# Optimization experiments

Hardware: AMD Instinct MI355X
Metric: run time of the kernel (lower is better)

The kernel has to match this reference:

```python
import jax, jax.numpy as jnp
import numpy as np

B, N, NUM_CLASS = 32, 4096, 40


def setup_inputs() -> dict:
    key = jax.random.key(0)
    ks = jax.random.split(key, 16)
    def w(k, o, i):
        return (jax.random.normal(k, (o, i), jnp.float32) / np.float32(np.sqrt(i)))
    inp = {"x": jax.random.uniform(ks[0], (B, N, 3), jnp.float32)}
    dims = [("sa1", 3, [64, 64, 128]), ("sa2", 3 + 128, [128, 128, 256]), ("sa3", 3 + 256, [256, 512, 1024])]
    ki = 1
    for name, cin, hs in dims:
        c = cin
        for j, h in enumerate(hs):
            inp[f"{name}_w{j}"] = w(jax.random.fold_in(ks[ki], j), h, c)
            inp[f"{name}_b{j}"] = jnp.zeros((h,), jnp.float32)
            c = h
        ki += 1
    for name, o, i in [("fc1", 512, 1024), ("fc2", 256, 512), ("fc3", NUM_CLASS, 256)]:
        inp[f"{name}_w"] = w(ks[ki], o, i)
        inp[f"{name}_b"] = jnp.zeros((o,), jnp.float32)
        ki += 1
    return inp


def _fps(xyz, npoint):
    # farthest point sampling for a single cloud, xyz: [N, 3] -> [npoint] indices
    n = xyz.shape[0]
    def body(carry, _):
        mind, last = carry
        d = jnp.sum((xyz - xyz[last]) ** 2, axis=-1)
        mind = jnp.minimum(mind, d)
        return (mind, jnp.argmax(mind).astype(jnp.int32)), last
    init = (jnp.full((n,), 1e10, xyz.dtype), jnp.int32(0))
    _, idx = jax.lax.scan(body, init, None, length=npoint)
    return idx


def _ball_query(new_xyz, xyz, radius, nsample):
    # new_xyz: [B,S,3], xyz: [B,N,3] -> [B,S,nsample] neighbor indices
    n = xyz.shape[1]
    sqd = (jnp.sum(new_xyz ** 2, -1)[:, :, None]
           + jnp.sum(xyz ** 2, -1)[:, None, :]
           - 2.0 * jnp.einsum('bsc,bnc->bsn', new_xyz, xyz))  # [B,S,N]
    gid = jnp.where(sqd <= radius ** 2, jnp.arange(n, dtype=jnp.int32), jnp.int32(n))
    gid = jnp.sort(gid, axis=-1)[..., :nsample]
    first = gid[..., :1]
    return jnp.where(gid == n, first, gid)


def _gather(x, idx):
    # x: [B,N,C], idx: [B,S,K] -> [B,S,K,C]
    return jax.vmap(lambda xb, ib: xb[ib])(x, idx)


def _shared_mlp(feat, layers):
    # feat: [..., C_in]; layers: list of (W [C_out,C_in], b [C_out]); 1x1 conv + ReLU (BN folded)
    for W, b in layers:
        feat = jax.nn.relu(jnp.einsum('bskc,oc->bsko', feat, W) + b)
    return feat


def _set_abstraction(xyz, feat, npoint, radius, nsample, layers):
    fidx = jax.vmap(lambda p: _fps(p, npoint))(xyz)            # [B,S]
    new_xyz = jax.vmap(lambda p, i: p[i])(xyz, fidx)           # [B,S,3]
    idx = _ball_query(new_xyz, xyz, radius, nsample)           # [B,S,K]
    gxyz = _gather(xyz, idx) - new_xyz[:, :, None, :]          # relative coords
    g = gxyz if feat is None else jnp.concatenate([gxyz, _gather(feat, idx)], axis=-1)
    g = _shared_mlp(g, layers)
    return new_xyz, jnp.max(g, axis=2)                         # max-pool over ball


def _sa_group_all(xyz, feat, layers):
    g = jnp.concatenate([xyz, feat], axis=-1)[:, None]         # [B,1,N,3+C]
    g = _shared_mlp(g, layers)
    return jnp.max(g, axis=2)[:, 0]                            # [B, 1024]


def reference(x,
              sa1_w0, sa1_b0, sa1_w1, sa1_b1, sa1_w2, sa1_b2,
              sa2_w0, sa2_b0, sa2_w1, sa2_b1, sa2_w2, sa2_b2,
              sa3_w0, sa3_b0, sa3_w1, sa3_b1, sa3_w2, sa3_b2,
              fc1_w, fc1_b, fc2_w, fc2_b, fc3_w, fc3_b):
    xyz, feat = x, None
    xyz, feat = _set_abstraction(xyz, feat, 512, 0.2, 32,
                                 [(sa1_w0, sa1_b0), (sa1_w1, sa1_b1), (sa1_w2, sa1_b2)])
    xyz, feat = _set_abstraction(xyz, feat, 128, 0.4, 64,
                                 [(sa2_w0, sa2_b0), (sa2_w1, sa2_b1), (sa2_w2, sa2_b2)])
    feat = _sa_group_all(xyz, feat,
                         [(sa3_w0, sa3_b0), (sa3_w1, sa3_b1), (sa3_w2, sa3_b2)])
    h = jax.nn.relu(feat @ fc1_w.T + fc1_b)
    h = jax.nn.relu(h @ fc2_w.T + fc2_b)
    logits = h @ fc3_w.T + fc3_b
    return jax.nn.softmax(logits, axis=-1)  # eval-mode output
```

## Files before the change

kernel.cpp:

```cpp
#include <hip/hip_runtime.h>
#include <math.h>

#define B_ 32
#define N_ 4096

typedef __attribute__((ext_vector_type(8))) short short8;
typedef __attribute__((ext_vector_type(4))) float f32x4;

__device__ __forceinline__ unsigned short f2bf(float f) {
    unsigned u = __float_as_uint(f);
    unsigned r = 0x7FFFu + ((u >> 16) & 1u);
    return (unsigned short)((u + r) >> 16);
}
__device__ __forceinline__ float bf2f(unsigned short h) {
    return __uint_as_float(((unsigned)h) << 16);
}
__device__ __forceinline__ void f2bfpair(float v, short& h, short& l) {
    unsigned short hh = f2bf(v);
    h = (short)hh;
    l = (short)f2bf(v - bf2f(hh));
}

__device__ __forceinline__ unsigned long long u64max(unsigned long long a,
                                                     unsigned long long b) {
    return a > b ? a : b;
}
template<int CTRL>
__device__ __forceinline__ unsigned long long dpp_u64(unsigned long long k) {
    int lo = __builtin_amdgcn_mov_dpp((int)(unsigned)k, CTRL, 0xf, 0xf, true);
    int hi = __builtin_amdgcn_mov_dpp((int)(unsigned)(k >> 32), CTRL, 0xf, 0xf, true);
    return ((unsigned long long)(unsigned)hi << 32) | (unsigned)lo;
}
__device__ __forceinline__ unsigned long long wave_argmax_u64(unsigned long long key) {
    key = u64max(key, dpp_u64<0x128>(key));
    key = u64max(key, dpp_u64<0x124>(key));
    key = u64max(key, dpp_u64<0x122>(key));
    key = u64max(key, dpp_u64<0x121>(key));
    key = u64max(key, __shfl_xor(key, 16));
    key = u64max(key, __shfl_xor(key, 32));
    return key;
}
__device__ __forceinline__ unsigned long long wave_argmax_u64_leader(unsigned long long key) {
    key = u64max(key, dpp_u64<0x128>(key));
    key = u64max(key, dpp_u64<0x124>(key));
    key = u64max(key, dpp_u64<0x122>(key));
    key = u64max(key, dpp_u64<0x121>(key));
    key = u64max(key, dpp_u64<0x142>(key));
    key = u64max(key, dpp_u64<0x143>(key));
    return key;
}

template<int N, int NPOINT, int NT>
__global__ __launch_bounds__(NT, 1) void fps_kernel(
    const float* __restrict__ xyz,
    int* __restrict__ outIdx,
    float* __restrict__ outXyz) {
#pragma clang fp contract(off)
    const int b = blockIdx.x;
    const int t = threadIdx.x;
    constexpr int PPT = N / NT;
    constexpr int NW = (NT + 63) / 64;
    __shared__ float ps[N][4];
    __shared__ unsigned long long red[2][NW];
    const float* base = xyz + (size_t)b * N * 3;
    for (int j = t; j < N; j += NT) {
        ps[j][0] = base[j * 3 + 0];
        ps[j][1] = base[j * 3 + 1];
        ps[j][2] = base[j * 3 + 2];
    }
    __syncthreads();
    float px[PPT], py[PPT], pz[PPT], mind[PPT];
    unsigned notp[PPT];
#pragma unroll
    for (int i = 0; i < PPT; i++) {
        int p = t + i * NT;
        f32x4 c4 = *(const f32x4*)&ps[p][0];
        px[i] = c4[0]; py[i] = c4[1]; pz[i] = c4[2];
        mind[i] = 1e10f;
        notp[i] = ~(unsigned)p;
    }
#pragma unroll
    for (int i = 0; i < PPT; i++)
        asm volatile("" : "+v"(px[i]), "+v"(py[i]), "+v"(pz[i]));
    float lx = ps[0][0], ly = ps[0][1], lz = ps[0][2];
    if (t == 0) {
        outIdx[b * NPOINT] = 0;
        outXyz[(size_t)b * NPOINT * 3 + 0] = lx;
        outXyz[(size_t)b * NPOINT * 3 + 1] = ly;
        outXyz[(size_t)b * NPOINT * 3 + 2] = lz;
    }
    for (int it = 1; it < NPOINT; it++) {
        unsigned long long key = 0;
#pragma unroll
        for (int i = 0; i < PPT; i++) {
            float dx = px[i] - lx, dy = py[i] - ly, dz = pz[i] - lz;
            float t0 = dx * dx, t1 = dy * dy, t2 = dz * dz;
            float d = (t0 + t1) + t2;
            float m = fminf(mind[i], d);
            mind[i] = m;
            unsigned long long k =
                ((unsigned long long)__float_as_uint(m) << 32) | notp[i];
            key = u64max(key, k);
        }
        int fi;
        if constexpr (NT > 64) {
            key = wave_argmax_u64_leader(key);
            const int par = it & 1;
            if ((t & 63) == 63) red[par][t >> 6] = key;
            __syncthreads();
            unsigned long long best = red[par][0];
#pragma unroll
            for (int w = 1; w < NW; w++) best = u64max(best, red[par][w]);
            fi = (int)(~(unsigned)best);
        } else {
            key = wave_argmax_u64(key);
            fi = (int)(~(unsigned)key);
        }
        f32x4 c4 = *(const f32x4*)&ps[fi][0];
        lx = c4[0]; ly = c4[1]; lz = c4[2];
        if (t == 0) {
            outIdx[b * NPOINT + it] = fi;
            outXyz[((size_t)b * NPOINT + it) * 3 + 0] = lx;
            outXyz[((size_t)b * NPOINT + it) * 3 + 1] = ly;
            outXyz[((size_t)b * NPOINT + it) * 3 + 2] = lz;
        }
    }
}

template<int N, int NS>
__global__ __launch_bounds__(256) void ballquery_kernel(
    const float* __restrict__ xyz, const float* __restrict__ newXyz,
    int* __restrict__ outIdx, int S, float r2) {
#pragma clang fp contract(off)
    const int qid = blockIdx.x * 4 + (threadIdx.x >> 6);
    const int lane = threadIdx.x & 63;
    const int b = qid / S;
    const float* q = newXyz + (size_t)qid * 3;
    const float qx = q[0], qy = q[1], qz = q[2];
    const float qn = (qx * qx + qy * qy) + qz * qz;
    const float* base = xyz + (size_t)b * N * 3;
    int* dst = outIdx + (size_t)qid * NS;
    int cnt = 0, first = 0;
    for (int p0 = 0; p0 < N; p0 += 64) {
        const int p = p0 + lane;
        const float x = base[p * 3 + 0];
        const float y = base[p * 3 + 1];
        const float z = base[p * 3 + 2];
        const float pn = (x * x + y * y) + z * z;
        const float dot = (qx * x + qy * y) + qz * z;
        const float sqd = (qn + pn) - 2.0f * dot;
        const unsigned long long mask = __ballot(sqd <= r2);
        if (mask) {
            if (cnt == 0) first = p0 + __ffsll((unsigned long long)mask) - 1;
            const int prefix = __builtin_amdgcn_mbcnt_hi(
                (unsigned)(mask >> 32),
                __builtin_amdgcn_mbcnt_lo((unsigned)mask, 0));
            const bool in = (mask >> lane) & 1ull;
            const int pos = cnt + prefix;
            if (in && pos < NS) dst[pos] = p;
            cnt += __popcll(mask);
            if (cnt >= NS) break;
        }
    }
    for (int i = cnt + lane; i < NS; i += 64) dst[i] = first;
}

struct WDesc { const float* src; short* dh; short* dl; int R, C, Cp, blk0, perm; };
struct WDescs { WDesc d[8]; };

__global__ void wprep_all_kernel(WDescs W) {
    const int blk = blockIdx.x;
    int di = 0;
#pragma unroll
    for (int k = 1; k < 8; k++) di = (blk >= W.d[k].blk0) ? k : di;
    const WDesc D = W.d[di];
    const int i = (blk - D.blk0) * 256 + threadIdx.x;
    if (i >= D.R * D.Cp) return;
    const int r = i / D.Cp, c = i % D.Cp;
    int cs;
    if (D.perm) cs = (c < 128) ? c + 3 : (c < 131 ? c - 128 : -1);
    else        cs = (c < D.C) ? c : -1;
    float v = (cs >= 0) ? D.src[r * D.C + cs] : 0.f;
    short h, l;
    f2bfpair(v, h, l);
    D.dh[i] = h; D.dl[i] = l;
}

template<int NT, int KS>
__device__ __forceinline__ void mfma_layer(
    const short* Aph, const short* Apl, const int sA,
    const short* __restrict__ Wph, const short* __restrict__ Wpl, const int sW,
    f32x4* acc, const int n0, const int mh, const int lr, const int lq) {
#pragma unroll
    for (int ks = 0; ks < KS; ks++) {
        const int ka = ks * 32 + lq * 8;
        short8 a_h[2], a_l[2];
#pragma unroll
        for (int mt = 0; mt < 2; mt++) {
            const int m = (mh * 2 + mt) * 16 + lr;
            a_h[mt] = *(const short8*)(Aph + m * sA + ka);
            a_l[mt] = *(const short8*)(Apl + m * sA + ka);
        }
#pragma unroll
        for (int nt = 0; nt < NT; nt++) {
            const int n = n0 + nt * 16 + lr;
            short8 b_h = *(const short8*)(Wph + (size_t)n * sW + ka);
            short8 b_l = *(const short8*)(Wpl + (size_t)n * sW + ka);
#pragma unroll
            for (int mt = 0; mt < 2; mt++) {
                f32x4 c = acc[mt * NT + nt];
                c = __builtin_amdgcn_mfma_f32_16x16x32_bf16(a_h[mt], b_h, c, 0, 0, 0);
                c = __builtin_amdgcn_mfma_f32_16x16x32_bf16(a_h[mt], b_l, c, 0, 0, 0);
                c = __builtin_amdgcn_mfma_f32_16x16x32_bf16(a_l[mt], b_h, c, 0, 0, 0);
                acc[mt * NT + nt] = c;
            }
        }
    }
}

template<int NT>
__device__ __forceinline__ void init_bias(f32x4* acc, const float* __restrict__ bias,
                                          const int n0, const int lr) {
#pragma unroll
    for (int nt = 0; nt < NT; nt++) {
        float bv = bias[n0 + nt * 16 + lr];
        f32x4 c = {bv, bv, bv, bv};
        acc[0 * NT + nt] = c;
        acc[1 * NT + nt] = c;
    }
}

template<int NT>
__device__ __forceinline__ void store_split(
    const f32x4* acc, short* Hp, short* Lp, const int stride,
    const int n0, const int mh, const int lr, const int lq) {
#pragma unroll
    for (int mt = 0; mt < 2; mt++)
#pragma unroll
        for (int nt = 0; nt < NT; nt++)
#pragma unroll
            for (int r = 0; r < 4; r++) {
                float v = fmaxf(acc[mt * NT + nt][r], 0.f);
                short h, l;
                f2bfpair(v, h, l);
                const int m = (mh * 2 + mt) * 16 + lq * 4 + r;
                const int n = n0 + nt * 16 + lr;
                Hp[m * stride + n] = h;
                Lp[m * stride + n] = l;
            }
}

#define T1 72
__global__ __launch_bounds__(256) void sa1_mfma_kernel(
    const float* __restrict__ x, const float* __restrict__ nxyz1,
    const int* __restrict__ idx,
    const float* __restrict__ w0, const float* __restrict__ b0,
    const short* __restrict__ w1h, const short* __restrict__ w1l,
    const float* __restrict__ b1,
    const short* __restrict__ w2h, const short* __restrict__ w2l,
    const float* __restrict__ b2,
    short* __restrict__ feat1h, short* __restrict__ feat1l) {
    const int g0 = blockIdx.x * 2;
    const int b = g0 >> 9;
    const int t = threadIdx.x;
    const int lane = t & 63, wv = t >> 6;
    const int lr = lane & 15, lq = lane >> 4;
    const int mh = wv & 1, nh = wv >> 1;
    __shared__ float gx[64][4];
    __shared__ short H1h[64 * T1], H1l[64 * T1];
    __shared__ short H2h[64 * T1], H2l[64 * T1];
    if (t < 64) {
        int g = g0 + (t >> 5);
        int id = idx[(size_t)g * 32 + (t & 31)];
        const float* pp = x + ((size_t)b * N_ + id) * 3;
        const float* cc = nxyz1 + (size_t)g * 3;
        gx[t][0] = pp[0] - cc[0];
        gx[t][1] = pp[1] - cc[1];
        gx[t][2] = pp[2] - cc[2];
    }
    __syncthreads();
    {
        const int m = t >> 2, oc = (t & 3) * 16;
        float a0 = gx[m][0], a1 = gx[m][1], a2 = gx[m][2];
        short8 hv0, hv1, lv0, lv1;
#pragma unroll
        for (int i = 0; i < 16; i++) {
            int o = oc + i;
            float v = fmaf(w0[o * 3 + 0], a0,
                      fmaf(w0[o * 3 + 1], a1,
                      fmaf(w0[o * 3 + 2], a2, b0[o])));
            v = fmaxf(v, 0.f);
            short h, l;
            f2bfpair(v, h, l);
            if (i < 8) { hv0[i] = h; lv0[i] = l; }
            else       { hv1[i - 8] = h; lv1[i - 8] = l; }
        }
        *(short8*)&H1h[m * T1 + oc]     = hv0;
        *(short8*)&H1h[m * T1 + oc + 8] = hv1;
        *(short8*)&H1l[m * T1 + oc]     = lv0;
        *(short8*)&H1l[m * T1 + oc + 8] = lv1;
    }
    __syncthreads();
    {
        f32x4 acc[4];
        init_bias<2>(acc, b1, nh * 32, lr);
        mfma_layer<2, 2>(H1h, H1l, T1, w1h, w1l, 64, acc, nh * 32, mh, lr, lq);
        store_split<2>(acc, H2h, H2l, T1, nh * 32, mh, lr, lq);
    }
    __syncthreads();
    {
        f32x4 acc[8];
        init_bias<4>(acc, b2, nh * 64, lr);
        mfma_layer<4, 2>(H2h, H2l, T1, w2h, w2l, 64, acc, nh * 64, mh, lr, lq);
#pragma unroll
        for (int nt = 0; nt < 4; nt++) {
            float v = 0.f;
#pragma unroll
            for (int mt = 0; mt < 2; mt++)
#pragma unroll
                for (int r = 0; r < 4; r++)
                    v = fmaxf(v, acc[mt * 4 + nt][r]);
            v = fmaxf(v, __shfl_xor(v, 16));
            v = fmaxf(v, __shfl_xor(v, 32));
            if (lane < 16) {
                short h, l;
                f2bfpair(v, h, l);
                size_t o = (size_t)(g0 + mh) * 128 + nh * 64 + nt * 16 + lane;
                feat1h[o] = h;
                feat1l[o] = l;
            }
        }
    }
}

#define S1 168
#define S2 136
__global__ __launch_bounds__(256) void sa2_mfma_kernel(
    const float* __restrict__ xyz1,
    const short* __restrict__ feat1h, const short* __restrict__ feat1l,
    const float* __restrict__ newXyz, const int* __restrict__ idx,
    const short* __restrict__ w0h, const short* __restrict__ w0l,
    const float* __restrict__ b0,
    const short* __restrict__ w1h, const short* __restrict__ w1l,
    const float* __restrict__ b1,
    const short* __restrict__ w2h, const short* __restrict__ w2l,
    const float* __restrict__ b2,
    short* __restrict__ a3h, short* __restrict__ a3l) {
    const int g = blockIdx.x;
    const int b = g >> 7;
    const int t = threadIdx.x;
    const int lane = t & 63, wv = t >> 6;
    const int lr = lane & 15, lq = lane >> 4;
    const int mh = wv & 1, nh = wv >> 1;
    __shared__ short Ah[64 * S1], Al[64 * S1];
    __shared__ short Hh[64 * S2], Hl[64 * S2];
    __shared__ float pmax[2][256];
    __shared__ int ids[64];
    if (t < 64) ids[t] = idx[(size_t)g * 64 + t];
    __syncthreads();
    {
        const int m = t >> 2, q = t & 3;
        const int id = ids[m];
        const size_t frow = ((size_t)b * 512 + id) * 128;
#pragma unroll
        for (int c8 = 0; c8 < 4; c8++) {
            const int k = q * 32 + c8 * 8;
            *(short8*)&Ah[m * S1 + k] = *(const short8*)(feat1h + frow + k);
            *(short8*)&Al[m * S1 + k] = *(const short8*)(feat1l + frow + k);
        }
        if (t < 64) {
            const int id2 = ids[t];
            short8 zz = {0, 0, 0, 0, 0, 0, 0, 0};
            *(short8*)&Ah[t * S1 + 128] = zz;
            *(short8*)&Ah[t * S1 + 136] = zz;
            *(short8*)&Ah[t * S1 + 144] = zz;
            *(short8*)&Ah[t * S1 + 152] = zz;
            *(short8*)&Al[t * S1 + 128] = zz;
            *(short8*)&Al[t * S1 + 136] = zz;
            *(short8*)&Al[t * S1 + 144] = zz;
            *(short8*)&Al[t * S1 + 152] = zz;
            const float* prow = xyz1 + ((size_t)b * 512 + id2) * 3;
            const float* crow = newXyz + (size_t)g * 3;
#pragma unroll
            for (int c = 0; c < 3; c++) {
                short h, l;
                f2bfpair(prow[c] - crow[c], h, l);
                Ah[t * S1 + 128 + c] = h;
                Al[t * S1 + 128 + c] = l;
            }
        }
    }
    __syncthreads();
    {
        f32x4 acc[8];
        init_bias<4>(acc, b0, nh * 64, lr);
        mfma_layer<4, 5>(Ah, Al, S1, w0h, w0l, 160, acc, nh * 64, mh, lr, lq);
        store_split<4>(acc, Hh, Hl, S2, nh * 64, mh, lr, lq);
    }
    __syncthreads();
    {
        f32x4 acc[8];
        init_bias<4>(acc, b1, nh * 64, lr);
        mfma_layer<4, 4>(Hh, Hl, S2, w1h, w1l, 128, acc, nh * 64, mh, lr, lq);
        store_split<4>(acc, Ah, Al, S2, nh * 64, mh, lr, lq);
    }
    __syncthreads();
    {
        f32x4 acc[16];
        init_bias<8>(acc, b2, nh * 128, lr);
        mfma_layer<8, 4>(Ah, Al, S2, w2h, w2l, 128, acc, nh * 128, mh, lr, lq);
#pragma unroll
        for (int nt = 0; nt < 8; nt++) {
            float v = 0.f;
#pragma unroll
            for (int mt = 0; mt < 2; mt++)
#pragma unroll
                for (int r = 0; r < 4; r++)
                    v = fmaxf(v, acc[mt * 8 + nt][r]);
            v = fmaxf(v, __shfl_xor(v, 16));
            v = fmaxf(v, __shfl_xor(v, 32));
            if (lane < 16) pmax[mh][nh * 128 + nt * 16 + lane] = v;
        }
    }
    __syncthreads();
    {
        float v = fmaxf(pmax[0][t], pmax[1][t]);
        short h, l;
        f2bfpair(v, h, l);
        a3h[(size_t)g * 288 + 3 + t] = h;
        a3l[(size_t)g * 288 + 3 + t] = l;
        if (t < 3) {
            f2bfpair(newXyz[(size_t)g * 3 + t], h, l);
            a3h[(size_t)g * 288 + t] = h;
            a3l[(size_t)g * 288 + t] = l;
        }
        if (t >= 227) {
            a3h[(size_t)g * 288 + t + 32] = 0;
            a3l[(size_t)g * 288 + t + 32] = 0;
        }
    }
}

template<int OUT_MODE>
__global__ __launch_bounds__(256) void mfma_gemm_kernel(
    const short* __restrict__ Agh, const short* __restrict__ Agl, const int Kp,
    const short* __restrict__ Wh, const short* __restrict__ Wl,
    const float* __restrict__ bias,
    float* __restrict__ outF, short* __restrict__ outH,
    short* __restrict__ outL, const int N) {
    const int t = threadIdx.x;
    const int lane = t & 63, wv = t >> 6;
    const int lr = lane & 15, lq = lane >> 4;
    const int mh = wv & 1, nh = wv >> 1;
    const int m0 = blockIdx.y * 64;
    const int n0 = blockIdx.x * 128 + nh * 64;
    __shared__ short Ah[64 * 40], Al[64 * 40];
    f32x4 acc[8];
#pragma unroll
    for (int nt = 0; nt < 4; nt++) {
        float bv = bias[n0 + nt * 16 + lr];
        f32x4 c = {bv, bv, bv, bv};
        acc[nt] = c; acc[4 + nt] = c;
    }
    const int srow = t >> 2, sk = (t & 3) * 8;
    for (int kt = 0; kt < Kp; kt += 32) {
        {
            const size_t src = (size_t)(m0 + srow) * Kp + kt + sk;
            *(short8*)&Ah[srow * 40 + sk] = *(const short8*)(Agh + src);
            *(short8*)&Al[srow * 40 + sk] = *(const short8*)(Agl + src);
        }
        __syncthreads();
        short8 a_h[2], a_l[2];
#pragma unroll
        for (int mt = 0; mt < 2; mt++) {
            const int m = mh * 32 + mt * 16 + lr;
            a_h[mt] = *(const short8*)&Ah[m * 40 + lq * 8];
            a_l[mt] = *(const short8*)&Al[m * 40 + lq * 8];
        }
#pragma unroll
        for (int nt = 0; nt < 4; nt++) {
            const int n = n0 + nt * 16 + lr;
            short8 b_h = *(const short8*)(Wh + (size_t)n * Kp + kt + lq * 8);
            short8 b_l = *(const short8*)(Wl + (size_t)n * Kp + kt + lq * 8);
#pragma unroll
            for (int mt = 0; mt < 2; mt++) {
                f32x4 c = acc[mt * 4 + nt];
                c = __builtin_amdgcn_mfma_f32_16x16x32_bf16(a_h[mt], b_h, c, 0, 0, 0);
                c = __builtin_amdgcn_mfma_f32_16x16x32_bf16(a_h[mt], b_l, c, 0, 0, 0);
                c = __builtin_amdgcn_mfma_f32_16x16x32_bf16(a_l[mt], b_h, c, 0, 0, 0);
                acc[mt * 4 + nt] = c;
            }
        }
        __syncthreads();
    }
    if (OUT_MODE == 2) {
        const int batch = blockIdx.y >> 1;
#pragma unroll
        for (int nt = 0; nt < 4; nt++) {
            float v = 0.f;
#pragma unroll
            for (int mt = 0; mt < 2; mt++)
#pragma unroll
                for (int r = 0; r < 4; r++)
                    v = fmaxf(v, acc[mt * 4 + nt][r]);
            v = fmaxf(v, __shfl_xor(v, 16));
            v = fmaxf(v, __shfl_xor(v, 32));
            if (lane < 16)
                atomicMax((int*)&outF[(size_t)batch * N + n0 + nt * 16 + lane],
                          __float_as_int(v));
        }
        return;
    }
#pragma unroll
    for (int mt = 0; mt < 2; mt++)
#pragma unroll
        for (int nt = 0; nt < 4; nt++)
#pragma unroll
            for (int r = 0; r < 4; r++) {
                const int m = m0 + mh * 32 + mt * 16 + lq * 4 + r;
                const int n = n0 + nt * 16 + lr;
                float v = fmaxf(acc[mt * 4 + nt][r], 0.f);
                short h, l;
                f2bfpair(v, h, l);
                outH[(size_t)m * N + n] = h;
                outL[(size_t)m * N + n] = l;
            }
}

template<int K, int OPW, int ACT>
__global__ __launch_bounds__(256) void fc_kernel(
    const float* __restrict__ in, const float* __restrict__ w,
    const float* __restrict__ bias, float* __restrict__ out, const int O) {
    const int batch = blockIdx.y;
    const int t = threadIdx.x, lane = t & 63, wv = t >> 6;
    __shared__ float f[K];
    for (int j = t; j < K; j += 256) f[j] = in[batch * K + j];
    __syncthreads();
    const int o0 = blockIdx.x * (4 * OPW) + wv * OPW;
#pragma unroll
    for (int i = 0; i < OPW; i++) {
        const int o = o0 + i;
        const float* wr = w + (size_t)o * K;
        float a = 0.f;
#pragma unroll
        for (int c = lane; c < K; c += 64) a = fmaf(wr[c], f[c], a);
#pragma unroll
        for (int off = 32; off > 0; off >>= 1) a += __shfl_xor(a, off);
        if (lane == 0) {
            float v = a + bias[o];
            out[batch * O + o] = ACT ? fmaxf(v, 0.f) : v;
        }
    }
}

__global__ __launch_bounds__(256) void fc3_softmax_kernel(
    const float* __restrict__ in, const float* __restrict__ w3,
    const float* __restrict__ b3, float* __restrict__ out) {
    const int b = blockIdx.x, t = threadIdx.x, lane = t & 63, wv = t >> 6;
    __shared__ float f[256];
    __shared__ float lg[40];
    f[t] = in[b * 256 + t];
    __syncthreads();
#pragma unroll
    for (int i = 0; i < 10; i++) {
        const int o = wv * 10 + i;
        const float* wr = w3 + (size_t)o * 256;
        float a = 0.f;
#pragma unroll
        for (int c = lane; c < 256; c += 64) a = fmaf(wr[c], f[c], a);
#pragma unroll
        for (int off = 32; off > 0; off >>= 1) a += __shfl_xor(a, off);
        if (lane == 0) lg[o] = a + b3[o];
    }
    __syncthreads();
    if (t < 64) {
        float v = (t < 40) ? lg[t] : -INFINITY;
        float m = v;
#pragma unroll
        for (int off = 32; off > 0; off >>= 1) m = fmaxf(m, __shfl_xor(m, off));
        float e = (t < 40) ? expf(v - m) : 0.f;
        float s = e;
#pragma unroll
        for (int off = 32; off > 0; off >>= 1) s += __shfl_xor(s, off);
        if (t < 40) out[b * 40 + t] = e / s;
    }
}

extern "C" void kernel_launch(void* const* d_in, const int* in_sizes, int n_in,
                              void* d_out, int out_size, void* d_ws, size_t ws_size,
                              hipStream_t stream) {
    (void)in_sizes; (void)n_in; (void)out_size; (void)ws_size;
    const float* x      = (const float*)d_in[0];
    const float* sa1w0  = (const float*)d_in[1];
    const float* sa1b0  = (const float*)d_in[2];
    const float* sa1w1  = (const float*)d_in[3];
    const float* sa1b1  = (const float*)d_in[4];
    const float* sa1w2  = (const float*)d_in[5];
    const float* sa1b2  = (const float*)d_in[6];
    const float* sa2w0  = (const float*)d_in[7];
    const float* sa2b0  = (const float*)d_in[8];
    const float* sa2w1  = (const float*)d_in[9];
    const float* sa2b1  = (const float*)d_in[10];
    const float* sa2w2  = (const float*)d_in[11];
    const float* sa2b2  = (const float*)d_in[12];
    const float* sa3w0  = (const float*)d_in[13];
    const float* sa3b0  = (const float*)d_in[14];
    const float* sa3w1  = (const float*)d_in[15];
    const float* sa3b1  = (const float*)d_in[16];
    const float* sa3w2  = (const float*)d_in[17];
    const float* sa3b2  = (const float*)d_in[18];
    const float* fc1w   = (const float*)d_in[19];
    const float* fc1b   = (const float*)d_in[20];
    const float* fc2w   = (const float*)d_in[21];
    const float* fc2b   = (const float*)d_in[22];
    const float* fc3w   = (const float*)d_in[23];
    const float* fc3b   = (const float*)d_in[24];
    float* outp = (float*)d_out;

    char* ws = (char*)d_ws;
    size_t off = 0;
    auto alloc = [&](size_t bytes) {
        void* p = ws + off;
        off += (bytes + 255) & ~(size_t)255;
        return p;
    };
    int*   fidx1   = (int*)  alloc((size_t)B_ * 512 * 4);
    float* nxyz1   = (float*)alloc((size_t)B_ * 512 * 3 * 4);
    int*   idx1    = (int*)  alloc((size_t)B_ * 512 * 32 * 4);
    short* feat1h  = (short*)alloc((size_t)B_ * 512 * 128 * 2);
    short* feat1l  = (short*)alloc((size_t)B_ * 512 * 128 * 2);
    int*   fidx2   = (int*)  alloc((size_t)B_ * 128 * 4);
    float* nxyz2   = (float*)alloc((size_t)B_ * 128 * 3 * 4);
    int*   idx2    = (int*)  alloc((size_t)B_ * 128 * 64 * 4);
    short* a3h     = (short*)alloc((size_t)4096 * 288 * 2);
    short* a3l     = (short*)alloc((size_t)4096 * 288 * 2);
    short* h3ah    = (short*)alloc((size_t)4096 * 256 * 2);
    short* h3al    = (short*)alloc((size_t)4096 * 256 * 2);
    short* h3bh    = (short*)alloc((size_t)4096 * 512 * 2);
    short* h3bl    = (short*)alloc((size_t)4096 * 512 * 2);
    float* gfeat   = (float*)alloc((size_t)B_ * 1024 * 4);
    float* h1      = (float*)alloc((size_t)B_ * 512 * 4);
    float* h2      = (float*)alloc((size_t)B_ * 256 * 4);
    short* w1h_s1 = (short*)alloc((size_t)64 * 64 * 2);
    short* w1l_s1 = (short*)alloc((size_t)64 * 64 * 2);
    short* w2h_s1 = (short*)alloc((size_t)128 * 64 * 2);
    short* w2l_s1 = (short*)alloc((size_t)128 * 64 * 2);
    short* w0h_s2 = (short*)alloc((size_t)128 * 160 * 2);
    short* w0l_s2 = (short*)alloc((size_t)128 * 160 * 2);
    short* w1h_s2 = (short*)alloc((size_t)128 * 128 * 2);
    short* w1l_s2 = (short*)alloc((size_t)128 * 128 * 2);
    short* w2h_s2 = (short*)alloc((size_t)256 * 128 * 2);
    short* w2l_s2 = (short*)alloc((size_t)256 * 128 * 2);
    short* w0h_s3 = (short*)alloc((size_t)256 * 288 * 2);
    short* w0l_s3 = (short*)alloc((size_t)256 * 288 * 2);
    short* w1h_s3 = (short*)alloc((size_t)512 * 256 * 2);
    short* w1l_s3 = (short*)alloc((size_t)512 * 256 * 2);
    short* w2h_s3 = (short*)alloc((size_t)1024 * 512 * 2);
    short* w2l_s3 = (short*)alloc((size_t)1024 * 512 * 2);

    {
        WDescs W;
        const float* srcs[8] = {sa1w1, sa1w2, sa2w0, sa2w1, sa2w2, sa3w0, sa3w1, sa3w2};
        short* dhs[8] = {w1h_s1, w2h_s1, w0h_s2, w1h_s2, w2h_s2, w0h_s3, w1h_s3, w2h_s3};
        short* dls[8] = {w1l_s1, w2l_s1, w0l_s2, w1l_s2, w2l_s2, w0l_s3, w1l_s3, w2l_s3};
        int Rs[8]  = {64, 128, 128, 128, 256, 256, 512, 1024};
        int Cs[8]  = {64, 64, 131, 128, 128, 259, 256, 512};
        int Cps[8] = {64, 64, 160, 128, 128, 288, 256, 512};
        int blk = 0;
        for (int k = 0; k < 8; k++) {
            W.d[k] = {srcs[k], dhs[k], dls[k], Rs[k], Cs[k], Cps[k], blk,
                      (k == 2) ? 1 : 0};
            blk += (Rs[k] * Cps[k] + 255) / 256;
        }
        wprep_all_kernel<<<blk, 256, 0, stream>>>(W);
    }
    hipMemsetAsync(gfeat, 0, (size_t)B_ * 1024 * 4, stream);

    fps_kernel<4096, 512, 256><<<B_, 256, 0, stream>>>(x, fidx1, nxyz1);
    ballquery_kernel<4096, 32><<<B_ * 512 / 4, 256, 0, stream>>>(
        x, nxyz1, idx1, 512, 0.04f);
    sa1_mfma_kernel<<<B_ * 512 / 2, 256, 0, stream>>>(
        x, nxyz1, idx1, sa1w0, sa1b0,
        w1h_s1, w1l_s1, sa1b1, w2h_s1, w2l_s1, sa1b2, feat1h, feat1l);
    fps_kernel<512, 128, 64><<<B_, 64, 0, stream>>>(nxyz1, fidx2, nxyz2);
    ballquery_kernel<512, 64><<<B_ * 128 / 4, 256, 0, stream>>>(
        nxyz1, nxyz2, idx2, 128, 0.16f);
    sa2_mfma_kernel<<<B_ * 128, 256, 0, stream>>>(
        nxyz1, feat1h, feat1l, nxyz2, idx2,
        w0h_s2, w0l_s2, sa2b0, w1h_s2, w1l_s2, sa2b1, w2h_s2, w2l_s2, sa2b2,
        a3h, a3l);
    mfma_gemm_kernel<1><<<dim3(2, 64), 256, 0, stream>>>(
        a3h, a3l, 288, w0h_s3, w0l_s3, sa3b0, nullptr, h3ah, h3al, 256);
    mfma_gemm_kernel<1><<<dim3(4, 64), 256, 0, stream>>>(
        h3ah, h3al, 256, w1h_s3, w1l_s3, sa3b1, nullptr, h3bh, h3bl, 512);
    mfma_gemm_kernel<2><<<dim3(8, 64), 256, 0, stream>>>(
        h3bh, h3bl, 512, w2h_s3, w2l_s3, sa3b2, gfeat, nullptr, nullptr, 1024);
    fc_kernel<1024, 16, 1><<<dim3(8, B_), 256, 0, stream>>>(
        gfeat, fc1w, fc1b, h1, 512);
    fc_kernel<512, 16, 1><<<dim3(4, B_), 256, 0, stream>>>(
        h1, fc2w, fc2b, h2, 256);
    fc3_softmax_kernel<<<B_, 256, 0, stream>>>(h2, fc3w, fc3b, outp);
}
```

Measured before the change: 1.032 ms.

## Co-schedule ball queries with second FPS and SA1 MLP in merged launches

The second-stage farthest point sampling only depends on the first FPS output, so it now runs as extra blocks of the first ball-query launch. The second ball query runs as extra blocks of the SA1 MLP launch. This removes two kernel launches and lets the serial, low-occupancy FPS2 overlap with independent ball-query and MLP work. Unused index outputs from FPS are also dropped. The cost is heterogeneous blocks inside one launch and a larger shared-memory footprint for the ball-query blocks, which may reduce occupancy.

```diff
diff --git a/kernel.cpp b/kernel.cpp
--- a/kernel.cpp
+++ b/kernel.cpp
@@ -52,9 +52,7 @@
 
 template<int N, int NPOINT, int NT>
 __global__ __launch_bounds__(NT, 1) void fps_kernel(
-    const float* __restrict__ xyz,
-    int* __restrict__ outIdx,
-    float* __restrict__ outXyz) {
+    const float* __restrict__ xyz, float* __restrict__ outXyz) {
 #pragma clang fp contract(off)
     const int b = blockIdx.x;
     const int t = threadIdx.x;
@@ -84,7 +82,6 @@
         asm volatile("" : "+v"(px[i]), "+v"(py[i]), "+v"(pz[i]));
     float lx = ps[0][0], ly = ps[0][1], lz = ps[0][2];
     if (t == 0) {
-        outIdx[b * NPOINT] = 0;
         outXyz[(size_t)b * NPOINT * 3 + 0] = lx;
         outXyz[(size_t)b * NPOINT * 3 + 1] = ly;
         outXyz[(size_t)b * NPOINT * 3 + 2] = lz;
@@ -102,24 +99,17 @@
                 ((unsigned long long)__float_as_uint(m) << 32) | notp[i];
             key = u64max(key, k);
         }
-        int fi;
-        if constexpr (NT > 64) {
-            key = wave_argmax_u64_leader(key);
-            const int par = it & 1;
-            if ((t & 63) == 63) red[par][t >> 6] = key;
-            __syncthreads();
-            unsigned long long best = red[par][0];
-#pragma unroll
-            for (int w = 1; w < NW; w++) best = u64max(best, red[par][w]);
-            fi = (int)(~(unsigned)best);
-        } else {
-            key = wave_argmax_u64(key);
-            fi = (int)(~(unsigned)key);
-        }
+        key = wave_argmax_u64_leader(key);
+        const int par = it & 1;
+        if ((t & 63) == 63) red[par][t >> 6] = key;
+        __syncthreads();
+        unsigned long long best = red[par][0];
+#pragma unroll
+        for (int w = 1; w < NW; w++) best = u64max(best, red[par][w]);
+        const int fi = (int)(~(unsigned)best);
         f32x4 c4 = *(const f32x4*)&ps[fi][0];
         lx = c4[0]; ly = c4[1]; lz = c4[2];
         if (t == 0) {
-            outIdx[b * NPOINT + it] = fi;
             outXyz[((size_t)b * NPOINT + it) * 3 + 0] = lx;
             outXyz[((size_t)b * NPOINT + it) * 3 + 1] = ly;
             outXyz[((size_t)b * NPOINT + it) * 3 + 2] = lz;
@@ -128,12 +118,10 @@
 }
 
 template<int N, int NS>
-__global__ __launch_bounds__(256) void ballquery_kernel(
+__device__ __forceinline__ void ballquery_body(
     const float* __restrict__ xyz, const float* __restrict__ newXyz,
-    int* __restrict__ outIdx, int S, float r2) {
+    int* __restrict__ outIdx, int S, float r2, int qid, int lane) {
 #pragma clang fp contract(off)
-    const int qid = blockIdx.x * 4 + (threadIdx.x >> 6);
-    const int lane = threadIdx.x & 63;
     const int b = qid / S;
     const float* q = newXyz + (size_t)qid * 3;
     const float qx = q[0], qy = q[1], qz = q[2];
@@ -165,6 +153,71 @@
     for (int i = cnt + lane; i < NS; i += 64) dst[i] = first;
 }
 
+template<int BQB, int NQ, int NS, int SQ, int NF, int NPF>
+__global__ __launch_bounds__(256) void bq_fps_kernel(
+    const float* __restrict__ xyzQ, const float* __restrict__ newXyzQ,
+    int* __restrict__ outIdxQ, float r2,
+    const float* __restrict__ xyzF, float* __restrict__ outXyzF) {
+#pragma clang fp contract(off)
+    const int t = threadIdx.x;
+    const int lane = t & 63, wv = t >> 6;
+    __shared__ float ps[NF][4];
+    if (blockIdx.x < BQB) {
+        ballquery_body<NQ, NS>(xyzQ, newXyzQ, outIdxQ, SQ, r2,
+                               blockIdx.x * 4 + wv, lane);
+        return;
+    }
+    const int b = blockIdx.x - BQB;
+    const float* base = xyzF + (size_t)b * NF * 3;
+    for (int j = t; j < NF; j += 256) {
+        ps[j][0] = base[j * 3 + 0];
+        ps[j][1] = base[j * 3 + 1];
+        ps[j][2] = base[j * 3 + 2];
+    }
+    __syncthreads();
+    if (t >= 64) return;
+    constexpr int PPT = NF / 64;
+    float px[PPT], py[PPT], pz[PPT], mind[PPT];
+    unsigned notp[PPT];
+#pragma unroll
+    for (int i = 0; i < PPT; i++) {
+        int p = t + i * 64;
+        f32x4 c4 = *(const f32x4*)&ps[p][0];
+        px[i] = c4[0]; py[i] = c4[1]; pz[i] = c4[2];
+        mind[i] = 1e10f;
+        notp[i] = ~(unsigned)p;
+    }
+    float lx = ps[0][0], ly = ps[0][1], lz = ps[0][2];
+    if (t == 0) {
+        outXyzF[(size_t)b * NPF * 3 + 0] = lx;
+        outXyzF[(size_t)b * NPF * 3 + 1] = ly;
+        outXyzF[(size_t)b * NPF * 3 + 2] = lz;
+    }
+    for (int it = 1; it < NPF; it++) {
+        unsigned long long key = 0;
+#pragma unroll
+        for (int i = 0; i < PPT; i++) {
+            float dx = px[i] - lx, dy = py[i] - ly, dz = pz[i] - lz;
+            float t0 = dx * dx, t1 = dy * dy, t2 = dz * dz;
+            float d = (t0 + t1) + t2;
+            float m = fminf(mind[i], d);
+            mind[i] = m;
+            unsigned long long k =
+                ((unsigned long long)__float_as_uint(m) << 32) | notp[i];
+            key = u64max(key, k);
+        }
+        key = wave_argmax_u64(key);
+        const int fi = (int)(~(unsigned)key);
+        f32x4 c4 = *(const f32x4*)&ps[fi][0];
+        lx = c4[0]; ly = c4[1]; lz = c4[2];
+        if (t == 0) {
+            outXyzF[((size_t)b * NPF + it) * 3 + 0] = lx;
+            outXyzF[((size_t)b * NPF + it) * 3 + 1] = ly;
+            outXyzF[((size_t)b * NPF + it) * 3 + 2] = lz;
+        }
+    }
+}
+
 struct WDesc { const float* src; short* dh; short* dl; int R, C, Cp, blk0, perm; };
 struct WDescs { WDesc d[8]; };
 
@@ -251,7 +304,8 @@
 }
 
 #define T1 72
-__global__ __launch_bounds__(256) void sa1_mfma_kernel(
+template<int SAB>
+__global__ __launch_bounds__(256) void sa1_bq2_kernel(
     const float* __restrict__ x, const float* __restrict__ nxyz1,
     const int* __restrict__ idx,
     const float* __restrict__ w0, const float* __restrict__ b0,
@@ -259,11 +313,17 @@
     const float* __restrict__ b1,
     const short* __restrict__ w2h, const short* __restrict__ w2l,
     const float* __restrict__ b2,
-    short* __restrict__ feat1h, short* __restrict__ feat1l) {
+    short* __restrict__ feat1h, short* __restrict__ feat1l,
+    const float* __restrict__ nxyz2, int* __restrict__ idx2, float r2q) {
+    const int t = threadIdx.x;
+    const int lane = t & 63, wv = t >> 6;
+    if (blockIdx.x >= SAB) {
+        ballquery_body<512, 64>(nxyz1, nxyz2, idx2, 128, r2q,
+                                (blockIdx.x - SAB) * 4 + wv, lane);
+        return;
+    }
     const int g0 = blockIdx.x * 2;
     const int b = g0 >> 9;
-    const int t = threadIdx.x;
-    const int lane = t & 63, wv = t >> 6;
     const int lr = lane & 15, lq = lane >> 4;
     const int mh = wv & 1, nh = wv >> 1;
     __shared__ float gx[64][4];
@@ -624,12 +684,10 @@
         off += (bytes + 255) & ~(size_t)255;
         return p;
     };
-    int*   fidx1   = (int*)  alloc((size_t)B_ * 512 * 4);
     float* nxyz1   = (float*)alloc((size_t)B_ * 512 * 3 * 4);
     int*   idx1    = (int*)  alloc((size_t)B_ * 512 * 32 * 4);
     short* feat1h  = (short*)alloc((size_t)B_ * 512 * 128 * 2);
     short* feat1l  = (short*)alloc((size_t)B_ * 512 * 128 * 2);
-    int*   fidx2   = (int*)  alloc((size_t)B_ * 128 * 4);
     float* nxyz2   = (float*)alloc((size_t)B_ * 128 * 3 * 4);
     int*   idx2    = (int*)  alloc((size_t)B_ * 128 * 64 * 4);
     short* a3h     = (short*)alloc((size_t)4096 * 288 * 2);
@@ -676,15 +734,14 @@
     }
     hipMemsetAsync(gfeat, 0, (size_t)B_ * 1024 * 4, stream);
 
-    fps_kernel<4096, 512, 256><<<B_, 256, 0, stream>>>(x, fidx1, nxyz1);
-    ballquery_kernel<4096, 32><<<B_ * 512 / 4, 256, 0, stream>>>(
-        x, nxyz1, idx1, 512, 0.04f);
-    sa1_mfma_kernel<<<B_ * 512 / 2, 256, 0, stream>>>(
+    fps_kernel<4096, 512, 256><<<B_, 256, 0, stream>>>(x, nxyz1);
+    bq_fps_kernel<4096, 4096, 32, 512, 512, 128>
+        <<<4096 + B_, 256, 0, stream>>>(
+            x, nxyz1, idx1, 0.04f, nxyz1, nxyz2);
+    sa1_bq2_kernel<8192><<<8192 + 1024, 256, 0, stream>>>(
         x, nxyz1, idx1, sa1w0, sa1b0,
-        w1h_s1, w1l_s1, sa1b1, w2h_s1, w2l_s1, sa1b2, feat1h, feat1l);
-    fps_kernel<512, 128, 64><<<B_, 64, 0, stream>>>(nxyz1, fidx2, nxyz2);
-    ballquery_kernel<512, 64><<<B_ * 128 / 4, 256, 0, stream>>>(
-        nxyz1, nxyz2, idx2, 128, 0.16f);
+        w1h_s1, w1l_s1, sa1b1, w2h_s1, w2l_s1, sa1b2, feat1h, feat1l,
+        nxyz2, idx2, 0.16f);
     sa2_mfma_kernel<<<B_ * 128, 256, 0, stream>>>(
         nxyz1, feat1h, feat1l, nxyz2, idx2,
         w0h_s2, w0l_s2, sa2b0, w1h_s2, w1l_s2, sa2b1, w2h_s2, w2l_s2, sa2b2,
```

New measurement: 0.9998 ms. 3.1% less time.
